# Performance work log

Measured on AMD Instinct MI355X. Metric: run time of the kernel, lower is better.

Reference implementation:

```python
import jax, jax.numpy as jnp
import numpy as np

B, S, C_IN, C_OUT = 8, 2048, 512, 512

def setup_inputs() -> dict:
    key = jax.random.key(0)
    k1, k2, k3, k4 = jax.random.split(key, 4)
    sc = 1.0 / np.sqrt(C_IN)
    return {
        "x": jax.random.normal(k1, (B, S, C_IN), dtype=jnp.float32),
        "Wq": jax.random.normal(k2, (C_OUT, C_IN), dtype=jnp.float32) * sc,
        "Wk": jax.random.normal(k3, (C_OUT, C_IN), dtype=jnp.float32) * sc,
        "Wv": jax.random.normal(k4, (C_OUT, C_IN), dtype=jnp.float32) * sc,
    }

def reference(x, Wq, Wk, Wv):
    # x: [B,S,Cin]; weights [Cout,Cin] (torch Linear convention, no bias)
    C = Wq.shape[0]
    dk = jnp.sqrt(jnp.float32(1.0) / C)  # torch: sqrt(1/out_features)
    q = jnp.einsum('bsi,oi->bso', x, Wq)
    k = jnp.einsum('bsi,oi->bso', x, Wk)
    v = jnp.einsum('bsi,oi->bso', x, Wv)
    phi_q = jax.nn.elu(q * dk) + 1.0
    phi_k = jax.nn.elu(k * dk) + 1.0
    b = x.shape[0]
    mem0 = jnp.zeros((b, C, C), x.dtype)   # running sum of phi_k v^T
    zeta0 = jnp.zeros((b, C), x.dtype)     # running sum of phi_k
    def step(carry, inp):
        mem, zeta = carry
        pq, pk, vv = inp                    # each [B,C]
        dm = pk[:, :, None] * vv[:, None, :]              # [B,C,C]
        scale = jnp.einsum('bc,bc->b', pq, pk + zeta) + 1e-5
        num = jnp.einsum('bc,bcd->bd', pq, dm + mem)
        y = num / scale[:, None]
        # state updates are under torch.no_grad -> detach
        new_mem = jax.lax.stop_gradient(mem + dm)
        new_zeta = jax.lax.stop_gradient(zeta + pk)
        return (new_mem, new_zeta), y
    xs = (phi_q.transpose(1, 0, 2), phi_k.transpose(1, 0, 2), v.transpose(1, 0, 2))
    _, ys = jax.lax.scan(step, (mem0, zeta0), xs)  # ys: [S,B,C]
    return ys.transpose(1, 0, 2)                   # [B,S,C]
```

## Files before the change

kernel.cpp:

```cpp
#include <hip/hip_runtime.h>


constexpr int Bn  = 8;
constexpr int Sn  = 2048;
constexpr int Cn  = 512;
constexpr int Tn  = 128;
constexpr int NCn = 16;
constexpr float DKf = 0.04419417382415922f;

typedef __attribute__((ext_vector_type(8))) short bf16x8;
typedef __attribute__((ext_vector_type(4))) float f32x4;

__device__ __forceinline__ unsigned short f2bf(float f) {
  unsigned u = __float_as_uint(f);
  u = (u + 0x7fffu + ((u >> 16) & 1u)) >> 16;
  return (unsigned short)u;
}
__device__ __forceinline__ float bf2f(unsigned short h) {
  return __uint_as_float(((unsigned)h) << 16);
}
__device__ __forceinline__ float phi_f(float u) {
  float s = u * DKf;
  return s > 0.0f ? s + 1.0f : __expf(s);
}

__device__ __forceinline__ void stage128x32(const unsigned short* __restrict__ g,
                                            int ld, unsigned short* lds,
                                            int wid, int lane) {
#pragma unroll
  for (int cc = 0; cc < 2; ++cc) {
    const int row = cc * 64 + wid * 16 + (lane >> 2);
    const int ks  = (lane & 3) ^ ((row >> 1) & 3);
    const unsigned short* src = g + (size_t)row * ld + ks * 8;
    unsigned short* dst = lds + (size_t)(cc * 256 + wid * 64) * 8;
    __builtin_amdgcn_global_load_lds(
        (const __attribute__((address_space(1))) void*)src,
        (__attribute__((address_space(3))) void*)dst, 16, 0, 0);
  }
}

__device__ __forceinline__ void mm_loop(const unsigned short* __restrict__ Ag, int lda,
                                        const unsigned short* __restrict__ Bg, int ldb,
                                        int nkt,
                                        unsigned short* Al, unsigned short* Bl,
                                        f32x4 acc[4][4]) {
  const int t = threadIdx.x, wid = t >> 6, lane = t & 63;
  const int wm = wid >> 1, wn = wid & 1;
  const int fr = lane & 15, kb = lane >> 4;
  stage128x32(Ag, lda, Al, wid, lane);
  stage128x32(Bg, ldb, Bl, wid, lane);
  int cur = 0;
  for (int kt = 0; kt < nkt; ++kt) {
    const int nxt = cur ^ 1;
    if (kt + 1 < nkt) {
      stage128x32(Ag + (kt + 1) * 32, lda, Al + nxt * 4096, wid, lane);
      stage128x32(Bg + (kt + 1) * 32, ldb, Bl + nxt * 4096, wid, lane);
      asm volatile("s_waitcnt vmcnt(4)" ::: "memory");
    } else {
      asm volatile("s_waitcnt vmcnt(0)" ::: "memory");
    }
    __builtin_amdgcn_s_barrier();
    asm volatile("" ::: "memory");
    const unsigned short* Ac = Al + cur * 4096;
    const unsigned short* Bc = Bl + cur * 4096;
    bf16x8 af[4], bf[4];
#pragma unroll
    for (int m = 0; m < 4; ++m) {
      const int r = wm * 64 + m * 16 + fr;
      af[m] = *(const bf16x8*)&Ac[r * 32 + ((kb ^ ((r >> 1) & 3)) << 3)];
    }
#pragma unroll
    for (int n = 0; n < 4; ++n) {
      const int r = wn * 64 + n * 16 + fr;
      bf[n] = *(const bf16x8*)&Bc[r * 32 + ((kb ^ ((r >> 1) & 3)) << 3)];
    }
#pragma unroll
    for (int m = 0; m < 4; ++m)
#pragma unroll
      for (int n = 0; n < 4; ++n)
        acc[m][n] = __builtin_amdgcn_mfma_f32_16x16x32_bf16(af[m], bf[n], acc[m][n], 0, 0, 0);
    __builtin_amdgcn_s_barrier();
    asm volatile("" ::: "memory");
    cur = nxt;
  }
}

__global__ __launch_bounds__(256) void k_cast_x(const float* __restrict__ x,
                                                unsigned short* __restrict__ xb) {
  const size_t i8 = ((size_t)blockIdx.x * 256 + threadIdx.x) * 8;
  float4 a = *(const float4*)&x[i8];
  float4 b = *(const float4*)&x[i8 + 4];
  uint4 o;
  o.x = (unsigned)f2bf(a.x) | ((unsigned)f2bf(a.y) << 16);
  o.y = (unsigned)f2bf(a.z) | ((unsigned)f2bf(a.w) << 16);
  o.z = (unsigned)f2bf(b.x) | ((unsigned)f2bf(b.y) << 16);
  o.w = (unsigned)f2bf(b.z) | ((unsigned)f2bf(b.w) << 16);
  *(uint4*)&xb[i8] = o;
}

__global__ __launch_bounds__(256) void k_cast_w(const float* __restrict__ Wq,
                                                const float* __restrict__ Wk,
                                                const float* __restrict__ Wv,
                                                unsigned short* __restrict__ Wb) {
  const int z = blockIdx.y;
  const float* __restrict__ src = (z == 0) ? Wq : (z == 1 ? Wk : Wv);
  const size_t i8 = ((size_t)blockIdx.x * 256 + threadIdx.x) * 8;
  float4 a = *(const float4*)&src[i8];
  float4 b = *(const float4*)&src[i8 + 4];
  uint4 o;
  o.x = (unsigned)f2bf(a.x) | ((unsigned)f2bf(a.y) << 16);
  o.y = (unsigned)f2bf(a.z) | ((unsigned)f2bf(a.w) << 16);
  o.z = (unsigned)f2bf(b.x) | ((unsigned)f2bf(b.y) << 16);
  o.w = (unsigned)f2bf(b.z) | ((unsigned)f2bf(b.w) << 16);
  *(uint4*)&Wb[(size_t)z * Cn * Cn + i8] = o;
}

__global__ __launch_bounds__(256) void k_proj(
    const unsigned short* __restrict__ xb, const unsigned short* __restrict__ Wb,
    unsigned short* __restrict__ PQ, unsigned short* __restrict__ PK,
    unsigned short* __restrict__ PKt, unsigned short* __restrict__ Vt,
    float* __restrict__ zsum)
{
  __shared__ unsigned short Al[2 * 128 * 32], Bl[2 * 128 * 32];
  __shared__ float zbuf[2][128];
  const int bid = blockIdx.x;
  const int xcd = bid & 7, idx = bid >> 3;
  const int n = idx & 3, z = (idx >> 2) % 3, mloc = idx / 12;
  const int n0 = n * 128, m0 = (xcd * 16 + mloc) * 128;
  const int t = threadIdx.x, wid = t >> 6, lane = t & 63;
  const int wm = wid >> 1, wn = wid & 1;
  f32x4 acc[4][4];
  const f32x4 zero = {0.f, 0.f, 0.f, 0.f};
#pragma unroll
  for (int m = 0; m < 4; ++m)
#pragma unroll
    for (int nn = 0; nn < 4; ++nn) acc[m][nn] = zero;

  mm_loop(xb + (size_t)m0 * Cn, Cn,
          Wb + (size_t)z * Cn * Cn + (size_t)n0 * Cn, Cn, Cn / 32, Al, Bl, acc);

  float ps[4] = {0.f, 0.f, 0.f, 0.f};
#pragma unroll
  for (int m = 0; m < 4; ++m)
#pragma unroll
    for (int nn = 0; nn < 4; ++nn) {
      const int row0 = m0 + wm * 64 + m * 16 + ((lane >> 4) << 2);
      const int col  = n0 + wn * 64 + nn * 16 + (lane & 15);
      f32x4 v = acc[m][nn];
      if (z == 0) {
#pragma unroll
        for (int j = 0; j < 4; ++j)
          PQ[(size_t)(row0 + j) * Cn + col] = f2bf(phi_f(v[j]));
      } else if (z == 1) {
        ushort4 p;
#pragma unroll
        for (int j = 0; j < 4; ++j) {
          unsigned short u = f2bf(phi_f(v[j]));
          PK[(size_t)(row0 + j) * Cn + col] = u;
          (&p.x)[j] = u;
          ps[nn] += bf2f(u);
        }
        const int b = row0 >> 11, tq = row0 & (Sn - 1);
        *(ushort4*)&PKt[((size_t)b * Cn + col) * Sn + tq] = p;
      } else {
        ushort4 p;
#pragma unroll
        for (int j = 0; j < 4; ++j) (&p.x)[j] = f2bf(v[j]);
        const int b = row0 >> 11, tq = row0 & (Sn - 1);
        *(ushort4*)&Vt[((size_t)b * Cn + col) * Sn + tq] = p;
      }
    }

  if (z == 1) {
#pragma unroll
    for (int nn = 0; nn < 4; ++nn) {
      float v = ps[nn];
      v += __shfl_xor(v, 16); v += __shfl_xor(v, 32);
      if (lane < 16) zbuf[wm][wn * 64 + nn * 16 + lane] = v;
    }
    __syncthreads();
    if (t < 128) {
      const int b = m0 >> 11, ch = (m0 >> 7) & 15;
      zsum[((size_t)b * NCn + ch) * Cn + n0 + t] = zbuf[0][t] + zbuf[1][t];
    }
  }
}

__global__ __launch_bounds__(256) void k_gram(
    const unsigned short* __restrict__ PQ, const unsigned short* __restrict__ PK,
    const float* __restrict__ zsum,
    unsigned short* __restrict__ Abuf, float* __restrict__ scale)
{
  __shared__ unsigned short Al[2 * 128 * 32], Bl[2 * 128 * 32];
  __shared__ float rsmem[2][128];
  __shared__ float zpl[512];
  const int b = blockIdx.y, ch = blockIdx.x;
  const size_t base = ((size_t)b * Sn + ch * Tn) * Cn;
  f32x4 acc[4][4];
  const f32x4 zero = {0.f, 0.f, 0.f, 0.f};
#pragma unroll
  for (int m = 0; m < 4; ++m)
#pragma unroll
    for (int n = 0; n < 4; ++n) acc[m][n] = zero;

  mm_loop(PQ + base, Cn, PK + base, Cn, Cn / 32, Al, Bl, acc);

  const int t = threadIdx.x, wid = t >> 6, lane = t & 63;
  const int wm = wid >> 1, wn = wid & 1;
  float rsum[4][4];
#pragma unroll
  for (int m = 0; m < 4; ++m)
#pragma unroll
    for (int j = 0; j < 4; ++j) rsum[m][j] = 0.f;
#pragma unroll
  for (int m = 0; m < 4; ++m)
#pragma unroll
    for (int n = 0; n < 4; ++n) {
      f32x4 v = acc[m][n];
#pragma unroll
      for (int j = 0; j < 4; ++j) {
        const int row = wm * 64 + m * 16 + ((lane >> 4) << 2) + j;
        const int col = wn * 64 + n * 16 + (lane & 15);
        unsigned short u = (col <= row) ? f2bf(v[j]) : 0;
        Abuf[((size_t)(b * NCn + ch) * Tn + row) * Tn + col] = u;
        rsum[m][j] += bf2f(u);
      }
    }
#pragma unroll
  for (int m = 0; m < 4; ++m)
#pragma unroll
    for (int j = 0; j < 4; ++j) {
      float r = rsum[m][j];
      r += __shfl_xor(r, 1); r += __shfl_xor(r, 2);
      r += __shfl_xor(r, 4); r += __shfl_xor(r, 8);
      if ((lane & 15) == 0)
        rsmem[wn][wm * 64 + m * 16 + ((lane >> 4) << 2) + j] = r;
    }
#pragma unroll
  for (int e = 0; e < 2; ++e) {
    const int c = t + e * 256;
    float s = 0.f;
    for (int ch2 = 0; ch2 < ch; ++ch2)
      s += zsum[((size_t)b * NCn + ch2) * Cn + c];
    zpl[c] = s;
  }
  __syncthreads();
  const int row = t >> 1, half = (t & 1) * 256;
  const unsigned short* pq = PQ + base + (size_t)row * Cn + half;
  float dacc = 0.f;
  for (int i = 0; i < 256; i += 8) {
    uint4 q = *(const uint4*)(pq + i);
    dacc += bf2f((unsigned short)(q.x & 0xffff)) * zpl[half + i + 0]
          + bf2f((unsigned short)(q.x >> 16))    * zpl[half + i + 1]
          + bf2f((unsigned short)(q.y & 0xffff)) * zpl[half + i + 2]
          + bf2f((unsigned short)(q.y >> 16))    * zpl[half + i + 3]
          + bf2f((unsigned short)(q.z & 0xffff)) * zpl[half + i + 4]
          + bf2f((unsigned short)(q.z >> 16))    * zpl[half + i + 5]
          + bf2f((unsigned short)(q.w & 0xffff)) * zpl[half + i + 6]
          + bf2f((unsigned short)(q.w >> 16))    * zpl[half + i + 7];
  }
  dacc += __shfl_xor(dacc, 1);
  if ((t & 1) == 0)
    scale[(size_t)b * Sn + ch * Tn + row] =
        rsmem[0][row] + rsmem[1][row] + dacc + 1e-5f;
}

__device__ __forceinline__ void stage64x128(const unsigned short* __restrict__ g,
                                            int ld, unsigned short* lds,
                                            int wid, int lane) {
#pragma unroll
  for (int i = 0; i < 4; ++i) {
    const int row = wid * 16 + i * 4 + (lane >> 4);
    const int s   = (lane & 15) ^ (row & 7);
    const unsigned short* src = g + (size_t)row * ld + s * 8;
    unsigned short* dst = lds + (size_t)(wid * 16 + i * 4) * 128;
    __builtin_amdgcn_global_load_lds(
        (const __attribute__((address_space(1))) void*)src,
        (__attribute__((address_space(3))) void*)dst, 16, 0, 0);
  }
}

__global__ __launch_bounds__(256) void k_kvp(
    const unsigned short* __restrict__ PKt, const unsigned short* __restrict__ Vt,
    unsigned short* __restrict__ Mpre)
{
  __shared__ unsigned short Al[2 * 64 * 128], Bl[2 * 64 * 128];
  const int bid = blockIdx.x;
  const int b = bid & 7, idx = bid >> 3;
  const int d0 = (idx & 7) * 64, c0 = (idx >> 3) * 64;
  const int t = threadIdx.x, wid = t >> 6, lane = t & 63;
  const int wm = wid >> 1, wn = wid & 1;
  const int fr = lane & 15, kb = lane >> 4;
  f32x4 acc[2][2];
  const f32x4 zero = {0.f, 0.f, 0.f, 0.f};
#pragma unroll
  for (int m = 0; m < 2; ++m)
#pragma unroll
    for (int n = 0; n < 2; ++n) acc[m][n] = zero;
  const unsigned short* Ag = PKt + ((size_t)b * Cn + c0) * Sn;
  const unsigned short* Bg = Vt  + ((size_t)b * Cn + d0) * Sn;
  stage64x128(Ag, Sn, Al, wid, lane);
  stage64x128(Bg, Sn, Bl, wid, lane);
  int cur = 0;
  for (int ch = 0; ch < NCn; ++ch) {
    const int nxt = cur ^ 1;
    if (ch + 1 < NCn) {
      stage64x128(Ag + (ch + 1) * Tn, Sn, Al + nxt * 8192, wid, lane);
      stage64x128(Bg + (ch + 1) * Tn, Sn, Bl + nxt * 8192, wid, lane);
      asm volatile("s_waitcnt vmcnt(8)" ::: "memory");
    } else {
      asm volatile("s_waitcnt vmcnt(0)" ::: "memory");
    }
    __builtin_amdgcn_s_barrier();
    asm volatile("" ::: "memory");
    if (ch > 0) {
#pragma unroll
      for (int m = 0; m < 2; ++m)
#pragma unroll
        for (int n = 0; n < 2; ++n) {
          const int c_row = c0 + wm * 32 + m * 16 + (kb << 2);
          const int d     = d0 + wn * 32 + n * 16 + fr;
          ushort4 p;
#pragma unroll
          for (int j = 0; j < 4; ++j) (&p.x)[j] = f2bf(acc[m][n][j]);
          *(ushort4*)&Mpre[((size_t)(b * NCn + ch) * Cn + d) * Cn + c_row] = p;
        }
    }
    const unsigned short* Ac = Al + cur * 8192;
    const unsigned short* Bc = Bl + cur * 8192;
#pragma unroll
    for (int kt = 0; kt < 4; ++kt) {
      bf16x8 af[2], bf[2];
#pragma unroll
      for (int m = 0; m < 2; ++m) {
        const int r = wm * 32 + m * 16 + fr;
        af[m] = *(const bf16x8*)&Ac[r * 128 + (((kt * 4 + kb) ^ (r & 7)) << 3)];
      }
#pragma unroll
      for (int n = 0; n < 2; ++n) {
        const int r = wn * 32 + n * 16 + fr;
        bf[n] = *(const bf16x8*)&Bc[r * 128 + (((kt * 4 + kb) ^ (r & 7)) << 3)];
      }
#pragma unroll
      for (int m = 0; m < 2; ++m)
#pragma unroll
        for (int n = 0; n < 2; ++n)
          acc[m][n] = __builtin_amdgcn_mfma_f32_16x16x32_bf16(af[m], bf[n], acc[m][n], 0, 0, 0);
    }
    __builtin_amdgcn_s_barrier();
    asm volatile("" ::: "memory");
    cur = nxt;
  }
}

__global__ __launch_bounds__(256) void k_avinter(
    const unsigned short* __restrict__ Abuf, const unsigned short* __restrict__ Vt,
    const unsigned short* __restrict__ PQ, const unsigned short* __restrict__ Mpre,
    const float* __restrict__ scale, float* __restrict__ out)
{
  __shared__ unsigned short Al[2 * 128 * 32], Bl[2 * 128 * 32];
  const int bid = blockIdx.x;
  const int logical = (bid & 7) * 64 + (bid >> 3);
  const int d0 = (logical & 3) * 128;
  const int ch = (logical >> 2) & 15;
  const int b  = logical >> 6;
  const int t0 = ch * Tn;
  f32x4 acc[4][4];
  const f32x4 zero = {0.f, 0.f, 0.f, 0.f};
#pragma unroll
  for (int m = 0; m < 4; ++m)
#pragma unroll
    for (int n = 0; n < 4; ++n) acc[m][n] = zero;

  mm_loop(Abuf + (size_t)(b * NCn + ch) * Tn * Tn, Tn,
          Vt + ((size_t)b * Cn + d0) * Sn + t0, Sn, Tn / 32, Al, Bl, acc);
  if (ch > 0)
    mm_loop(PQ + ((size_t)b * Sn + t0) * Cn, Cn,
            Mpre + ((size_t)(b * NCn + ch) * Cn + d0) * Cn, Cn, Cn / 32, Al, Bl, acc);

  const int t = threadIdx.x, wid = t >> 6, lane = t & 63;
  const int wm = wid >> 1, wn = wid & 1;
#pragma unroll
  for (int m = 0; m < 4; ++m)
#pragma unroll
    for (int n = 0; n < 4; ++n) {
      const int row0 = t0 + wm * 64 + m * 16 + ((lane >> 4) << 2);
      const int col  = d0 + wn * 64 + n * 16 + (lane & 15);
      f32x4 v = acc[m][n];
#pragma unroll
      for (int j = 0; j < 4; ++j) {
        const size_t sidx = (size_t)b * Sn + row0 + j;
        out[sidx * Cn + col] = v[j] / scale[sidx];
      }
    }
}

extern "C" void kernel_launch(void* const* d_in, const int* in_sizes, int n_in,
                              void* d_out, int out_size, void* d_ws, size_t ws_size,
                              hipStream_t stream)
{
  const float* x  = (const float*)d_in[0];
  const float* Wq = (const float*)d_in[1];
  const float* Wk = (const float*)d_in[2];
  const float* Wv = (const float*)d_in[3];
  float* out = (float*)d_out;

  unsigned short* xb   = (unsigned short*)d_ws;
  unsigned short* Wb   = xb   + (size_t)Bn * Sn * Cn;
  unsigned short* PQ   = Wb   + (size_t)3 * Cn * Cn;
  unsigned short* PK   = PQ   + (size_t)Bn * Sn * Cn;
  unsigned short* PKt  = PK   + (size_t)Bn * Sn * Cn;
  unsigned short* Vt   = PKt  + (size_t)Bn * Sn * Cn;
  unsigned short* Abuf = Vt   + (size_t)Bn * Sn * Cn;
  unsigned short* Mpre = Abuf + (size_t)Bn * NCn * Tn * Tn;
  float* scale = (float*)(Mpre + (size_t)Bn * NCn * Cn * Cn);
  float* zsum  = scale + (size_t)Bn * Sn;
  (void)ws_size; (void)in_sizes; (void)n_in; (void)out_size;

  hipLaunchKernelGGL(k_cast_x, dim3(4096), dim3(256), 0, stream, x, xb);
  hipLaunchKernelGGL(k_cast_w, dim3(128, 3), dim3(256), 0, stream, Wq, Wk, Wv, Wb);
  hipLaunchKernelGGL(k_proj, dim3(1536), dim3(256), 0, stream, xb, Wb, PQ, PK, PKt, Vt, zsum);
  hipLaunchKernelGGL(k_gram, dim3(NCn, Bn), dim3(256), 0, stream, PQ, PK, zsum, Abuf, scale);
  hipLaunchKernelGGL(k_kvp, dim3(512), dim3(256), 0, stream, PKt, Vt, Mpre);
  hipLaunchKernelGGL(k_avinter, dim3(512), dim3(256), 0, stream, Abuf, Vt, PQ, Mpre, scale, out);
}
```

Baseline: 133.9 us.

## Give each wave private LDS staging to drop block barriers in matmul loops

Each wave now stages its own 64-row A and B slices into a private LDS region and double-buffers there, so the per-k-step workgroup s_barrier pairs are removed from all GEMM loops (proj, gram, state, avinter). MFMA sections are wrapped with s_setprio to favor compute-issuing waves. The cost is duplicated global/LDS traffic, since waves sharing rows or columns each load them separately, and LDS use per block grows to 64KB, which may reduce occupancy.

```diff
diff --git a/kernel.cpp b/kernel.cpp
--- a/kernel.cpp
+++ b/kernel.cpp
@@ -24,63 +24,56 @@
   return s > 0.0f ? s + 1.0f : __expf(s);
 }
 
-__device__ __forceinline__ void stage128x32(const unsigned short* __restrict__ g,
-                                            int ld, unsigned short* lds,
-                                            int wid, int lane) {
-#pragma unroll
-  for (int cc = 0; cc < 2; ++cc) {
-    const int row = cc * 64 + wid * 16 + (lane >> 2);
+__device__ __forceinline__ void stage64x32w(const unsigned short* __restrict__ g,
+                                            int ld, unsigned short* lds, int lane) {
+#pragma unroll
+  for (int i = 0; i < 4; ++i) {
+    const int row = i * 16 + (lane >> 2);
     const int ks  = (lane & 3) ^ ((row >> 1) & 3);
-    const unsigned short* src = g + (size_t)row * ld + ks * 8;
-    unsigned short* dst = lds + (size_t)(cc * 256 + wid * 64) * 8;
     __builtin_amdgcn_global_load_lds(
-        (const __attribute__((address_space(1))) void*)src,
-        (__attribute__((address_space(3))) void*)dst, 16, 0, 0);
-  }
-}
-
-__device__ __forceinline__ void mm_loop(const unsigned short* __restrict__ Ag, int lda,
-                                        const unsigned short* __restrict__ Bg, int ldb,
-                                        int nkt,
-                                        unsigned short* Al, unsigned short* Bl,
-                                        f32x4 acc[4][4]) {
-  const int t = threadIdx.x, wid = t >> 6, lane = t & 63;
-  const int wm = wid >> 1, wn = wid & 1;
+        (const __attribute__((address_space(1))) void*)(g + (size_t)row * ld + ks * 8),
+        (__attribute__((address_space(3))) void*)(lds + i * 512), 16, 0, 0);
+  }
+}
+
+__device__ __forceinline__ void wmm_loop(const unsigned short* __restrict__ Ag, int lda,
+                                         const unsigned short* __restrict__ Bg, int ldb,
+                                         int nkt, unsigned short* wbase,
+                                         f32x4 acc[4][4]) {
+  const int lane = threadIdx.x & 63;
   const int fr = lane & 15, kb = lane >> 4;
-  stage128x32(Ag, lda, Al, wid, lane);
-  stage128x32(Bg, ldb, Bl, wid, lane);
+  stage64x32w(Ag, lda, wbase, lane);
+  stage64x32w(Bg, ldb, wbase + 2048, lane);
   int cur = 0;
   for (int kt = 0; kt < nkt; ++kt) {
     const int nxt = cur ^ 1;
     if (kt + 1 < nkt) {
-      stage128x32(Ag + (kt + 1) * 32, lda, Al + nxt * 4096, wid, lane);
-      stage128x32(Bg + (kt + 1) * 32, ldb, Bl + nxt * 4096, wid, lane);
-      asm volatile("s_waitcnt vmcnt(4)" ::: "memory");
+      stage64x32w(Ag + (kt + 1) * 32, lda, wbase + nxt * 4096, lane);
+      stage64x32w(Bg + (kt + 1) * 32, ldb, wbase + nxt * 4096 + 2048, lane);
+      asm volatile("s_waitcnt vmcnt(8)" ::: "memory");
     } else {
       asm volatile("s_waitcnt vmcnt(0)" ::: "memory");
     }
-    __builtin_amdgcn_s_barrier();
-    asm volatile("" ::: "memory");
-    const unsigned short* Ac = Al + cur * 4096;
-    const unsigned short* Bc = Bl + cur * 4096;
+    const unsigned short* Ac = wbase + cur * 4096;
+    const unsigned short* Bc = Ac + 2048;
     bf16x8 af[4], bf[4];
 #pragma unroll
     for (int m = 0; m < 4; ++m) {
-      const int r = wm * 64 + m * 16 + fr;
+      const int r = m * 16 + fr;
       af[m] = *(const bf16x8*)&Ac[r * 32 + ((kb ^ ((r >> 1) & 3)) << 3)];
     }
 #pragma unroll
     for (int n = 0; n < 4; ++n) {
-      const int r = wn * 64 + n * 16 + fr;
+      const int r = n * 16 + fr;
       bf[n] = *(const bf16x8*)&Bc[r * 32 + ((kb ^ ((r >> 1) & 3)) << 3)];
     }
+    __builtin_amdgcn_s_setprio(1);
 #pragma unroll
     for (int m = 0; m < 4; ++m)
 #pragma unroll
       for (int n = 0; n < 4; ++n)
         acc[m][n] = __builtin_amdgcn_mfma_f32_16x16x32_bf16(af[m], bf[n], acc[m][n], 0, 0, 0);
-    __builtin_amdgcn_s_barrier();
-    asm volatile("" ::: "memory");
+    __builtin_amdgcn_s_setprio(0);
     cur = nxt;
   }
 }
@@ -121,7 +114,7 @@
     unsigned short* __restrict__ PKt, unsigned short* __restrict__ Vt,
     float* __restrict__ zsum)
 {
-  __shared__ unsigned short Al[2 * 128 * 32], Bl[2 * 128 * 32];
+  __shared__ unsigned short smem[4 * 8192];
   __shared__ float zbuf[2][128];
   const int bid = blockIdx.x;
   const int xcd = bid & 7, idx = bid >> 3;
@@ -136,8 +129,9 @@
 #pragma unroll
     for (int nn = 0; nn < 4; ++nn) acc[m][nn] = zero;
 
-  mm_loop(xb + (size_t)m0 * Cn, Cn,
-          Wb + (size_t)z * Cn * Cn + (size_t)n0 * Cn, Cn, Cn / 32, Al, Bl, acc);
+  wmm_loop(xb + (size_t)(m0 + wm * 64) * Cn, Cn,
+           Wb + (size_t)z * Cn * Cn + (size_t)(n0 + wn * 64) * Cn, Cn,
+           Cn / 32, smem + wid * 8192, acc);
 
   float ps[4] = {0.f, 0.f, 0.f, 0.f};
 #pragma unroll
@@ -191,11 +185,13 @@
     const float* __restrict__ zsum,
     unsigned short* __restrict__ Abuf, float* __restrict__ scale)
 {
-  __shared__ unsigned short Al[2 * 128 * 32], Bl[2 * 128 * 32];
+  __shared__ unsigned short smem[4 * 8192];
   __shared__ float rsmem[2][128];
   __shared__ float zpl[512];
   const int b = blockIdx.y, ch = blockIdx.x;
   const size_t base = ((size_t)b * Sn + ch * Tn) * Cn;
+  const int t = threadIdx.x, wid = t >> 6, lane = t & 63;
+  const int wm = wid >> 1, wn = wid & 1;
   f32x4 acc[4][4];
   const f32x4 zero = {0.f, 0.f, 0.f, 0.f};
 #pragma unroll
@@ -203,10 +199,10 @@
 #pragma unroll
     for (int n = 0; n < 4; ++n) acc[m][n] = zero;
 
-  mm_loop(PQ + base, Cn, PK + base, Cn, Cn / 32, Al, Bl, acc);
-
-  const int t = threadIdx.x, wid = t >> 6, lane = t & 63;
-  const int wm = wid >> 1, wn = wid & 1;
+  wmm_loop(PQ + base + (size_t)(wm * 64) * Cn, Cn,
+           PK + base + (size_t)(wn * 64) * Cn, Cn,
+           Cn / 32, smem + wid * 8192, acc);
+
   float rsum[4][4];
 #pragma unroll
   for (int m = 0; m < 4; ++m)
@@ -265,18 +261,15 @@
         rsmem[0][row] + rsmem[1][row] + dacc + 1e-5f;
 }
 
-__device__ __forceinline__ void stage64x128(const unsigned short* __restrict__ g,
-                                            int ld, unsigned short* lds,
-                                            int wid, int lane) {
+__device__ __forceinline__ void stage32x64w(const unsigned short* __restrict__ g,
+                                            int ld, unsigned short* lds, int lane) {
 #pragma unroll
   for (int i = 0; i < 4; ++i) {
-    const int row = wid * 16 + i * 4 + (lane >> 4);
-    const int s   = (lane & 15) ^ (row & 7);
-    const unsigned short* src = g + (size_t)row * ld + s * 8;
-    unsigned short* dst = lds + (size_t)(wid * 16 + i * 4) * 128;
+    const int row = i * 8 + (lane >> 3);
+    const int ks  = (lane & 7) ^ (row & 7);
     __builtin_amdgcn_global_load_lds(
-        (const __attribute__((address_space(1))) void*)src,
-        (__attribute__((address_space(3))) void*)dst, 16, 0, 0);
+        (const __attribute__((address_space(1))) void*)(g + (size_t)row * ld + ks * 8),
+        (__attribute__((address_space(3))) void*)(lds + i * 512), 16, 0, 0);
   }
 }
 
@@ -284,36 +277,29 @@
     const unsigned short* __restrict__ PKt, const unsigned short* __restrict__ Vt,
     unsigned short* __restrict__ Mpre)
 {
-  __shared__ unsigned short Al[2 * 64 * 128], Bl[2 * 64 * 128];
+  __shared__ unsigned short smem[4 * 8192];
   const int bid = blockIdx.x;
   const int b = bid & 7, idx = bid >> 3;
   const int d0 = (idx & 7) * 64, c0 = (idx >> 3) * 64;
   const int t = threadIdx.x, wid = t >> 6, lane = t & 63;
   const int wm = wid >> 1, wn = wid & 1;
   const int fr = lane & 15, kb = lane >> 4;
+  unsigned short* wbase = smem + wid * 8192;
   f32x4 acc[2][2];
   const f32x4 zero = {0.f, 0.f, 0.f, 0.f};
 #pragma unroll
   for (int m = 0; m < 2; ++m)
 #pragma unroll
     for (int n = 0; n < 2; ++n) acc[m][n] = zero;
-  const unsigned short* Ag = PKt + ((size_t)b * Cn + c0) * Sn;
-  const unsigned short* Bg = Vt  + ((size_t)b * Cn + d0) * Sn;
-  stage64x128(Ag, Sn, Al, wid, lane);
-  stage64x128(Bg, Sn, Bl, wid, lane);
+  const unsigned short* Ag = PKt + ((size_t)b * Cn + c0 + wm * 32) * Sn;
+  const unsigned short* Bg = Vt  + ((size_t)b * Cn + d0 + wn * 32) * Sn;
+  stage32x64w(Ag, Sn, wbase, lane);
+  stage32x64w(Bg, Sn, wbase + 2048, lane);
   int cur = 0;
-  for (int ch = 0; ch < NCn; ++ch) {
+  for (int kt = 0; kt < 32; ++kt) {
     const int nxt = cur ^ 1;
-    if (ch + 1 < NCn) {
-      stage64x128(Ag + (ch + 1) * Tn, Sn, Al + nxt * 8192, wid, lane);
-      stage64x128(Bg + (ch + 1) * Tn, Sn, Bl + nxt * 8192, wid, lane);
-      asm volatile("s_waitcnt vmcnt(8)" ::: "memory");
-    } else {
-      asm volatile("s_waitcnt vmcnt(0)" ::: "memory");
-    }
-    __builtin_amdgcn_s_barrier();
-    asm volatile("" ::: "memory");
-    if (ch > 0) {
+    if ((kt & 1) == 0 && kt > 0) {
+      const int ch = kt >> 1;
 #pragma unroll
       for (int m = 0; m < 2; ++m)
 #pragma unroll
@@ -326,20 +312,28 @@
           *(ushort4*)&Mpre[((size_t)(b * NCn + ch) * Cn + d) * Cn + c_row] = p;
         }
     }
-    const unsigned short* Ac = Al + cur * 8192;
-    const unsigned short* Bc = Bl + cur * 8192;
-#pragma unroll
-    for (int kt = 0; kt < 4; ++kt) {
+    if (kt + 1 < 32) {
+      stage32x64w(Ag + (kt + 1) * 64, Sn, wbase + nxt * 4096, lane);
+      stage32x64w(Bg + (kt + 1) * 64, Sn, wbase + nxt * 4096 + 2048, lane);
+      asm volatile("s_waitcnt vmcnt(8)" ::: "memory");
+    } else {
+      asm volatile("s_waitcnt vmcnt(0)" ::: "memory");
+    }
+    const unsigned short* Ac = wbase + cur * 4096;
+    const unsigned short* Bc = Ac + 2048;
+    __builtin_amdgcn_s_setprio(1);
+#pragma unroll
+    for (int kk = 0; kk < 2; ++kk) {
       bf16x8 af[2], bf[2];
 #pragma unroll
       for (int m = 0; m < 2; ++m) {
-        const int r = wm * 32 + m * 16 + fr;
-        af[m] = *(const bf16x8*)&Ac[r * 128 + (((kt * 4 + kb) ^ (r & 7)) << 3)];
+        const int r = m * 16 + fr;
+        af[m] = *(const bf16x8*)&Ac[r * 64 + (((kk * 4 + kb) ^ (r & 7)) << 3)];
       }
 #pragma unroll
       for (int n = 0; n < 2; ++n) {
-        const int r = wn * 32 + n * 16 + fr;
-        bf[n] = *(const bf16x8*)&Bc[r * 128 + (((kt * 4 + kb) ^ (r & 7)) << 3)];
+        const int r = n * 16 + fr;
+        bf[n] = *(const bf16x8*)&Bc[r * 64 + (((kk * 4 + kb) ^ (r & 7)) << 3)];
       }
 #pragma unroll
       for (int m = 0; m < 2; ++m)
@@ -347,8 +341,7 @@
         for (int n = 0; n < 2; ++n)
           acc[m][n] = __builtin_amdgcn_mfma_f32_16x16x32_bf16(af[m], bf[n], acc[m][n], 0, 0, 0);
     }
-    __builtin_amdgcn_s_barrier();
-    asm volatile("" ::: "memory");
+    __builtin_amdgcn_s_setprio(0);
     cur = nxt;
   }
 }
@@ -358,13 +351,16 @@
     const unsigned short* __restrict__ PQ, const unsigned short* __restrict__ Mpre,
     const float* __restrict__ scale, float* __restrict__ out)
 {
-  __shared__ unsigned short Al[2 * 128 * 32], Bl[2 * 128 * 32];
+  __shared__ unsigned short smem[4 * 8192];
   const int bid = blockIdx.x;
   const int logical = (bid & 7) * 64 + (bid >> 3);
   const int d0 = (logical & 3) * 128;
   const int ch = (logical >> 2) & 15;
   const int b  = logical >> 6;
   const int t0 = ch * Tn;
+  const int t = threadIdx.x, wid = t >> 6, lane = t & 63;
+  const int wm = wid >> 1, wn = wid & 1;
+  unsigned short* wbase = smem + wid * 8192;
   f32x4 acc[4][4];
   const f32x4 zero = {0.f, 0.f, 0.f, 0.f};
 #pragma unroll
@@ -372,14 +368,14 @@
 #pragma unroll
     for (int n = 0; n < 4; ++n) acc[m][n] = zero;
 
-  mm_loop(Abuf + (size_t)(b * NCn + ch) * Tn * Tn, Tn,
-          Vt + ((size_t)b * Cn + d0) * Sn + t0, Sn, Tn / 32, Al, Bl, acc);
+  wmm_loop(Abuf + (size_t)(b * NCn + ch) * Tn * Tn + (size_t)(wm * 64) * Tn, Tn,
+           Vt + ((size_t)b * Cn + d0 + wn * 64) * Sn + t0, Sn,
+           Tn / 32, wbase, acc);
   if (ch > 0)
-    mm_loop(PQ + ((size_t)b * Sn + t0) * Cn, Cn,
-            Mpre + ((size_t)(b * NCn + ch) * Cn + d0) * Cn, Cn, Cn / 32, Al, Bl, acc);
-
-  const int t = threadIdx.x, wid = t >> 6, lane = t & 63;
-  const int wm = wid >> 1, wn = wid & 1;
+    wmm_loop(PQ + ((size_t)b * Sn + t0 + wm * 64) * Cn, Cn,
+             Mpre + ((size_t)(b * NCn + ch) * Cn + d0 + wn * 64) * Cn, Cn,
+             Cn / 32, wbase, acc);
+
 #pragma unroll
   for (int m = 0; m < 4; ++m)
 #pragma unroll
```

Result: slower. 150.3 us (+12.3%).
